# Performance work log

Measured on AMD Instinct MI355X. Metric: run time of the kernel, lower is better.

## Reference

```python
import jax, jax.numpy as jnp
import numpy as np

L = 2; B = 16; H = 56; W = 56; N = H * W; D = 256
HEADS = 8; HD = 32; INNER = HEADS * HD
WIN = 7; WIN2 = WIN * WIN; NWH = H // WIN; NWW = W // WIN; NW = NWH * NWW
DISP = WIN // 2; FF = 4 * D; CPB = 512; EPS = 1e-5


def _shift_masks():
    d = DISP
    ul = np.zeros((WIN2, WIN2), np.float32)
    ul[-d * WIN:, :-d * WIN] = -np.inf
    ul[:-d * WIN, -d * WIN:] = -np.inf
    lr = np.zeros((WIN, WIN, WIN, WIN), np.float32)
    lr[:, -d:, :, :-d] = -np.inf
    lr[:, :-d, :, -d:] = -np.inf
    return jnp.asarray(ul), jnp.asarray(lr.reshape(WIN2, WIN2))

MASK_UL, MASK_LR = _shift_masks()

_idx = np.array([[i, j] for i in range(WIN) for j in range(WIN)], np.float32)
_rel = _idx[None, :, :] - _idx[:, None, :]  # (49,49,2) relative distances
REL = jnp.asarray((np.sign(_rel) * np.log1p(np.abs(_rel))).reshape(WIN2 * WIN2, 2))


def _ln(x, g, b):
    m = x.mean(-1, keepdims=True)
    v = ((x - m) ** 2).mean(-1, keepdims=True)
    return (x - m) / jnp.sqrt(v + EPS) * g + b


def _l2norm(t):
    return t / jnp.maximum(jnp.linalg.norm(t, axis=-1, keepdims=True), 1e-12)


def _window_attn(xm, qkv_w, tau, cw1, cb1, cw2, cb2, ow, ob, shifted):
    if shifted:
        xm = jnp.roll(xm, (-DISP, -DISP), (1, 2))
    qkv = xm @ qkv_w  # (B,H,W,3*INNER), no bias
    q, k, v = jnp.split(qkv, 3, axis=-1)

    def towin(t):  # (B,H,W,INNER) -> (B,heads,nw,win2,hd)
        t = t.reshape(B, NWH, WIN, NWW, WIN, HEADS, HD)
        return t.transpose(0, 5, 1, 3, 2, 4, 6).reshape(B, HEADS, NW, WIN2, HD)

    q, k, v = towin(q), towin(k), towin(v)
    # cosine-similarity attention
    dots = jnp.einsum('bhwid,bhwjd->bhwij', _l2norm(q), _l2norm(k))
    dots = dots / jnp.clip(tau, 0.01, None)[None, :, None, None, None]
    # continuous position bias MLP: 2 -> CPB -> heads
    cpb = (jax.nn.relu(REL @ cw1 + cb1) @ cw2 + cb2).reshape(WIN2, WIN2, HEADS)
    dots = dots + cpb.transpose(2, 0, 1)[None, :, None]
    if shifted:
        dots = dots.at[:, :, -NWW:].add(MASK_UL)
        dots = dots.at[:, :, NWW - 1::NWW].add(MASK_LR)
    attn = jax.nn.softmax(dots, -1)
    out = jnp.einsum('bhwij,bhwjd->bhwid', attn, v)
    out = out.reshape(B, HEADS, NWH, NWW, WIN, WIN, HD)
    out = out.transpose(0, 2, 4, 3, 5, 1, 6).reshape(B, H, W, INNER)
    out = out @ ow + ob
    if shifted:
        out = jnp.roll(out, (DISP, DISP), (1, 2))
    return out


def _forward(x, spe, qkv_w, tau, cw1, cb1, cw2, cb2, ow, ob, ln1_g, ln1_b,
             fw1, fb1, fw2, fb2, ln2_g, ln2_b, norm_g, norm_b):
    xm = (x + spe).reshape(B, H, W, D)
    for i in range(L):
        shifted = (i % 2 == 1)
        a = _window_attn(xm, qkv_w[i], tau[i], cw1[i], cb1[i], cw2[i], cb2[i],
                         ow[i], ob[i], shifted)
        xm = _ln(a, ln1_g[i], ln1_b[i]) + xm  # Residual(PostNorm(attn))
        f = jax.nn.gelu(xm @ fw1[i] + fb1[i], approximate=False) @ fw2[i] + fb2[i]
        xm = _ln(f, ln2_g[i], ln2_b[i]) + xm  # Residual(PostNorm(mlp))
    return _ln(xm, norm_g, norm_b).reshape(B, N, D)


def setup_inputs():
    key = jax.random.key(0)
    ks = jax.random.split(key, 10)
    rn = lambda k, shp, s: jax.random.normal(k, shp, jnp.float32) * s
    return {
        'x': rn(ks[0], (B, N, D), 1.0),
        'spatial_position_embedding': rn(ks[1], (B, N, D), 0.02),
        'qkv_w': rn(ks[2], (L, D, 3 * INNER), 0.02),
        'tau': jnp.ones((L, HEADS), jnp.float32),
        'cw1': rn(ks[3], (L, 2, CPB), 0.1),
        'cb1': jnp.zeros((L, CPB), jnp.float32),
        'cw2': rn(ks[4], (L, CPB, HEADS), 0.05),
        'cb2': jnp.zeros((L, HEADS), jnp.float32),
        'ow': rn(ks[5], (L, INNER, D), 0.02),
        'ob': jnp.zeros((L, D), jnp.float32),
        'ln1_g': jnp.ones((L, D), jnp.float32),
        'ln1_b': jnp.zeros((L, D), jnp.float32),
        'fw1': rn(ks[6], (L, D, FF), 0.02),
        'fb1': jnp.zeros((L, FF), jnp.float32),
        'fw2': rn(ks[7], (L, FF, D), 0.02),
        'fb2': jnp.zeros((L, D), jnp.float32),
        'ln2_g': jnp.ones((L, D), jnp.float32),
        'ln2_b': jnp.zeros((L, D), jnp.float32),
        'norm_g': jnp.ones((D,), jnp.float32),
        'norm_b': jnp.zeros((D,), jnp.float32),
    }


def reference(x, spatial_position_embedding, qkv_w, tau, cw1, cb1, cw2, cb2, ow, ob,
              ln1_g, ln1_b, fw1, fb1, fw2, fb2, ln2_g, ln2_b, norm_g, norm_b):
    return _forward(x, spatial_position_embedding, qkv_w, tau, cw1, cb1, cw2, cb2,
                    ow, ob, ln1_g, ln1_b, fw1, fb1, fw2, fb2, ln2_g, ln2_b,
                    norm_g, norm_b)
```

## Files before the change

kernel.cpp:

```cpp
#include <hip/hip_runtime.h>
#include <hip/hip_bf16.h>
#include <math.h>

typedef short    short8  __attribute__((ext_vector_type(8)));
typedef float    floatx4 __attribute__((ext_vector_type(4)));

__device__ __forceinline__ float b2f(unsigned short u) {
    union { float f; unsigned int i; } v; v.i = ((unsigned int)u) << 16; return v.f;
}
__device__ __forceinline__ unsigned short f2b(float f) {
    union { float f; unsigned int i; } v; v.f = f;
    unsigned int b = v.i;
    return (unsigned short)((b + 0x7FFFu + ((b >> 16) & 1u)) >> 16);
}
__device__ __forceinline__ float rd(const void* p, long i, int f) {
    return f ? ((const float*)p)[i] : b2f(((const unsigned short*)p)[i]);
}
__device__ __forceinline__ float fgelu(float x) {
    float x2 = x * x;
    float t = x * fmaf(x2, -0.0713548163f, -1.5957691216f);
    return __fdividef(x, 1.f + __expf(t));
}
__device__ __forceinline__ int xcd_swz(int bid, int nwg) {
    int q = nwg >> 3, r = nwg & 7;
    int xcd = bid & 7, loc = bid >> 3;
    return ((xcd < r) ? xcd * (q + 1) : r * (q + 1) + (xcd - r) * q) + loc;
}

#define NTOK_ 50176

__global__ __launch_bounds__(256) void k_detect(const unsigned short* __restrict__ x,
                                                int* __restrict__ flag) {
    __shared__ int cnt;
    if (threadIdx.x == 0) cnt = 0;
    __syncthreads();
    unsigned short v = x[threadIdx.x];
    int e = (v >> 7) & 0xFF;
    if (e >= 0x90) atomicAdd(&cnt, 1);
    __syncthreads();
    if (threadIdx.x == 0) *flag = (cnt >= 8) ? 1 : 0;
}

__global__ __launch_bounds__(256) void k_add_spe(const void* __restrict__ x,
                                                 const void* __restrict__ spe,
                                                 float* __restrict__ xm,
                                                 unsigned short* __restrict__ xb,
                                                 const int* __restrict__ flagp) {
    const int f = *flagp;
    long i = ((long)blockIdx.x * 256 + threadIdx.x) * 4;
    float4 o;
    if (f) {
        float4 a = *(const float4*)((const float*)x + i);
        float4 b = *(const float4*)((const float*)spe + i);
        o.x = a.x + b.x; o.y = a.y + b.y; o.z = a.z + b.z; o.w = a.w + b.w;
    } else {
        ushort4 a = *(const ushort4*)((const unsigned short*)x + i);
        ushort4 b = *(const ushort4*)((const unsigned short*)spe + i);
        o.x = b2f(a.x) + b2f(b.x); o.y = b2f(a.y) + b2f(b.y);
        o.z = b2f(a.z) + b2f(b.z); o.w = b2f(a.w) + b2f(b.w);
    }
    *(float4*)(xm + i) = o;
    if (xb) {
        ushort4 h; h.x = f2b(o.x); h.y = f2b(o.y); h.z = f2b(o.z); h.w = f2b(o.w);
        *(ushort4*)(xb + i) = h;
    }
}

__global__ __launch_bounds__(256) void k_transpose(const void* __restrict__ in, long ioff,
                                                   unsigned short* __restrict__ out,
                                                   int K, int N,
                                                   const int* __restrict__ flagp) {
    __shared__ unsigned short tile[32][33];
    const int f = *flagp;
    int n0 = blockIdx.x * 32, k0 = blockIdx.y * 32;
    int tx = threadIdx.x & 31, ty = threadIdx.x >> 5;
#pragma unroll
    for (int i = 0; i < 4; i++) {
        int k = k0 + ty + i * 8;
        long idx = ioff + (long)k * N + n0 + tx;
        unsigned short v = f ? f2b(((const float*)in)[idx])
                             : ((const unsigned short*)in)[idx];
        tile[ty + i * 8][tx] = v;
    }
    __syncthreads();
#pragma unroll
    for (int i = 0; i < 4; i++) {
        int n = n0 + ty + i * 8;
        out[(long)n * K + k0 + tx] = tile[tx][ty + i * 8];
    }
}

__global__ __launch_bounds__(512) void k_cpb(const void* __restrict__ cw1,
                                             const void* __restrict__ cb1,
                                             const void* __restrict__ cw2,
                                             const void* __restrict__ cb2,
                                             float* __restrict__ cpb,
                                             const int* __restrict__ flagp) {
    const int f = *flagp;
    int p = blockIdx.x;
    int l = blockIdx.y;
    int t = threadIdx.x;
    int i = p / 49, j = p - i * 49;
    int yi = i / 7, xi = i - yi * 7, yj = j / 7, xj = j - yj * 7;
    float dy = (float)(yj - yi), dx = (float)(xj - xi);
    float sy = (dy > 0.f) ? 1.f : ((dy < 0.f) ? -1.f : 0.f);
    float sx = (dx > 0.f) ? 1.f : ((dx < 0.f) ? -1.f : 0.f);
    float r0 = sy * log1pf(fabsf(dy));
    float r1 = sx * log1pf(fabsf(dx));
    float h = r0 * rd(cw1, l * 1024 + t, f) + r1 * rd(cw1, l * 1024 + 512 + t, f)
            + rd(cb1, l * 512 + t, f);
    h = fmaxf(h, 0.f);
    __shared__ float red[512];
    for (int hh = 0; hh < 8; hh++) {
        red[t] = h * rd(cw2, (long)(l * 512 + t) * 8 + hh, f);
        __syncthreads();
        for (int s = 256; s > 0; s >>= 1) {
            if (t < s) red[t] += red[t + s];
            __syncthreads();
        }
        if (t == 0) cpb[((long)l * 8 + hh) * 2401 + p] = red[0] + rd(cb2, l * 8 + hh, f);
        __syncthreads();
    }
}

__global__ __launch_bounds__(256) void k_cast_roll(const float* __restrict__ xmg,
                                                   unsigned short* __restrict__ xb, int shift) {
    int gid = blockIdx.x * 256 + threadIdx.x;
    int c4 = (gid & 63) * 4;
    int t = gid >> 6;
    int x = t % 56; int t2 = t / 56;
    int y = t2 % 56;
    int b = t2 / 56;
    int ys = y + shift; if (ys >= 56) ys -= 56;
    int xs = x + shift; if (xs >= 56) xs -= 56;
    float4 v = *(const float4*)(xmg + (((long)b * 3136 + ys * 56 + xs) * 256 + c4));
    ushort4 o; o.x = f2b(v.x); o.y = f2b(v.y); o.z = f2b(v.z); o.w = f2b(v.w);
    *(ushort4*)(xb + ((long)t * 256 + c4)) = o;
}

__global__ __launch_bounds__(256) void gemm_bt(const unsigned short* __restrict__ A,
                                               const unsigned short* __restrict__ Bt,
                                               const void* __restrict__ bias, long boff,
                                               void* __restrict__ Cp,
                                               int M, int N, int K, int flags,
                                               const int* __restrict__ flagp) {
    __shared__ __align__(16) unsigned short smem[16896];
    unsigned short* As = smem;
    const int f = *flagp;
    const int tid = threadIdx.x;
    const int lane = tid & 63;
    const int wave = tid >> 6;
    const int wrow = (wave >> 1) * 64;
    const int wcol = (wave & 1) * 64;

    const int nwg = gridDim.x * gridDim.y;
    const int nb = xcd_swz(blockIdx.y * gridDim.x + blockIdx.x, nwg);
    const int bn = nb % gridDim.x, bm = nb / gridDim.x;

    floatx4 acc[4][4] = {};

    const int arow = tid >> 2;
    const int aseg = (tid & 3) * 8;
    const unsigned short* Ag = A + (long)(bm * 128 + arow) * K + aseg;
    const long rstep = (long)64 * K;

    const int q = lane >> 4;
    const int mrow = lane & 15;

    const unsigned short* Brow[4];
#pragma unroll
    for (int nt = 0; nt < 4; nt++)
        Brow[nt] = Bt + (long)(bn * 128 + wcol + nt * 16 + mrow) * K + q * 8;

    uint4 a_cur0 = *(const uint4*)(Ag);
    uint4 a_cur1 = *(const uint4*)(Ag + rstep);
    short8 bf_cur[4], bf_nxt[4];
#pragma unroll
    for (int nt = 0; nt < 4; nt++) bf_cur[nt] = *(const short8*)(Brow[nt]);

    for (int k0 = 0; k0 < K; k0 += 32) {
        const int kn = k0 + 32;
        uint4 a_nxt0, a_nxt1;
        if (kn < K) {
            a_nxt0 = *(const uint4*)(Ag + kn);
            a_nxt1 = *(const uint4*)(Ag + kn + rstep);
#pragma unroll
            for (int nt = 0; nt < 4; nt++) bf_nxt[nt] = *(const short8*)(Brow[nt] + kn);
        }
        __syncthreads();
        *(uint4*)(As + arow * 40 + aseg) = a_cur0;
        *(uint4*)(As + (arow + 64) * 40 + aseg) = a_cur1;
        __syncthreads();

        short8 af_[4];
#pragma unroll
        for (int mt = 0; mt < 4; mt++)
            af_[mt] = *(const short8*)(As + (wrow + mt * 16 + mrow) * 40 + q * 8);
#pragma unroll
        for (int mt = 0; mt < 4; mt++)
#pragma unroll
            for (int nt = 0; nt < 4; nt++)
                acc[mt][nt] = __builtin_amdgcn_mfma_f32_16x16x32_bf16(af_[mt], bf_cur[nt], acc[mt][nt], 0, 0, 0);
        if (kn < K) {
            a_cur0 = a_nxt0; a_cur1 = a_nxt1;
#pragma unroll
            for (int nt = 0; nt < 4; nt++) bf_cur[nt] = bf_nxt[nt];
        }
    }

    __syncthreads();

    unsigned short* T = smem;
#pragma unroll
    for (int nt = 0; nt < 4; nt++) {
        int col = wcol + nt * 16 + mrow;
        float bv = (flags & 1) ? rd(bias, boff + bn * 128 + col, f) : 0.f;
#pragma unroll
        for (int mt = 0; mt < 4; mt++) {
            int row0 = wrow + mt * 16 + q * 4;
#pragma unroll
            for (int r = 0; r < 4; r++) {
                float v = acc[mt][nt][r] + bv;
                if (flags & 2) v = fgelu(v);
                T[(row0 + r) * 132 + col] = f2b(v);
            }
        }
    }
    __syncthreads();
    unsigned short* Cu = (unsigned short*)Cp;
    int row = tid >> 4;
    int col8 = (tid & 15) * 8;
#pragma unroll
    for (int p = 0; p < 8; p++) {
        int rr = p * 16 + row;
        *(uint4*)(Cu + (long)(bm * 128 + rr) * N + bn * 128 + col8) =
            *(const uint4*)(T + rr * 132 + col8);
    }
}

__global__ __launch_bounds__(256) void gemm_ln(const unsigned short* __restrict__ A,
                                               const unsigned short* __restrict__ Bt,
                                               const void* __restrict__ bias, long boff,
                                               const void* __restrict__ g, long goff,
                                               const void* __restrict__ bb, long b2off,
                                               float* __restrict__ xm,
                                               unsigned short* __restrict__ xb,
                                               int K, int xbmode,
                                               const void* __restrict__ fg,
                                               const void* __restrict__ fb,
                                               void* __restrict__ outp,
                                               const int* __restrict__ flagp) {
    __shared__ __align__(16) unsigned short smem[17152];
    __shared__ float pp[4][32][2];
    unsigned short* As = smem;
    unsigned short* Bs = smem + 1280;
    const int f = *flagp;
    const int tid = threadIdx.x;
    const int lane = tid & 63;
    const int wv = tid >> 6;
    const int wcol = wv * 64;
    const int bm = blockIdx.x;

    floatx4 acc[2][4] = {};
    const int brow = tid >> 2;
    const int bseg = (tid & 3) * 8;
    const unsigned short* Ag = A + (long)(bm * 32 + brow) * K + bseg;
    const unsigned short* Bg = Bt + (long)brow * K + bseg;
    const long brow2 = (long)64 * K;
    const int q = lane >> 4;
    const int c = lane & 15;

    for (int k0 = 0; k0 < K; k0 += 32) {
        uint4 a0;
        if (tid < 128) a0 = *(const uint4*)(Ag + k0);
        uint4 b0 = *(const uint4*)(Bg + k0);
        uint4 b1 = *(const uint4*)(Bg + k0 + brow2);
        uint4 b2 = *(const uint4*)(Bg + k0 + 2 * brow2);
        uint4 b3 = *(const uint4*)(Bg + k0 + 3 * brow2);
        __syncthreads();
        if (tid < 128) *(uint4*)(As + brow * 40 + bseg) = a0;
        *(uint4*)(Bs + brow * 40 + bseg) = b0;
        *(uint4*)(Bs + (brow + 64) * 40 + bseg) = b1;
        *(uint4*)(Bs + (brow + 128) * 40 + bseg) = b2;
        *(uint4*)(Bs + (brow + 192) * 40 + bseg) = b3;
        __syncthreads();

        short8 af_[2], bf_[4];
#pragma unroll
        for (int mt = 0; mt < 2; mt++)
            af_[mt] = *(const short8*)(As + (mt * 16 + c) * 40 + q * 8);
#pragma unroll
        for (int nt = 0; nt < 4; nt++)
            bf_[nt] = *(const short8*)(Bs + (wcol + nt * 16 + c) * 40 + q * 8);
#pragma unroll
        for (int mt = 0; mt < 2; mt++)
#pragma unroll
            for (int nt = 0; nt < 4; nt++)
                acc[mt][nt] = __builtin_amdgcn_mfma_f32_16x16x32_bf16(af_[mt], bf_[nt], acc[mt][nt], 0, 0, 0);
    }
    __syncthreads();

    float bv[4];
#pragma unroll
    for (int nt = 0; nt < 4; nt++)
        bv[nt] = rd(bias, boff + wcol + nt * 16 + c, f);
#pragma unroll
    for (int mt = 0; mt < 2; mt++) {
#pragma unroll
        for (int r = 0; r < 4; r++) {
            float s1 = 0.f, s2 = 0.f;
#pragma unroll
            for (int nt = 0; nt < 4; nt++) {
                float v = acc[mt][nt][r] + bv[nt];
                s1 += v; s2 += v * v;
            }
            s1 += __shfl_xor(s1, 1); s2 += __shfl_xor(s2, 1);
            s1 += __shfl_xor(s1, 2); s2 += __shfl_xor(s2, 2);
            s1 += __shfl_xor(s1, 4); s2 += __shfl_xor(s2, 4);
            s1 += __shfl_xor(s1, 8); s2 += __shfl_xor(s2, 8);
            if (c == 0) {
                pp[wv][mt * 16 + q * 4 + r][0] = s1;
                pp[wv][mt * 16 + q * 4 + r][1] = s2;
            }
        }
    }

    const int c0 = lane * 4;
    float4 gv, bbv, fgv, fbv;
    gv.x = rd(g, goff + c0 + 0, f); gv.y = rd(g, goff + c0 + 1, f);
    gv.z = rd(g, goff + c0 + 2, f); gv.w = rd(g, goff + c0 + 3, f);
    bbv.x = rd(bb, b2off + c0 + 0, f); bbv.y = rd(bb, b2off + c0 + 1, f);
    bbv.z = rd(bb, b2off + c0 + 2, f); bbv.w = rd(bb, b2off + c0 + 3, f);
    if (xbmode == 3) {
        fgv.x = rd(fg, c0 + 0, f); fgv.y = rd(fg, c0 + 1, f);
        fgv.z = rd(fg, c0 + 2, f); fgv.w = rd(fg, c0 + 3, f);
        fbv.x = rd(fb, c0 + 0, f); fbv.y = rd(fb, c0 + 1, f);
        fbv.z = rd(fb, c0 + 2, f); fbv.w = rd(fb, c0 + 3, f);
    }

    float* Tf = (float*)smem;
#pragma unroll
    for (int mt = 0; mt < 2; mt++)
#pragma unroll
        for (int nt = 0; nt < 4; nt++)
#pragma unroll
            for (int r = 0; r < 4; r++)
                Tf[(mt * 16 + q * 4 + r) * 268 + wcol + nt * 16 + c] = acc[mt][nt][r] + bv[nt];
    __syncthreads();
#pragma unroll
    for (int it = 0; it < 8; it++) {
        int row = wv * 8 + it;
        float sum = pp[0][row][0] + pp[1][row][0] + pp[2][row][0] + pp[3][row][0];
        float ssq = pp[0][row][1] + pp[1][row][1] + pp[2][row][1] + pp[3][row][1];
        float mean = sum * (1.f / 256.f);
        float var = ssq * (1.f / 256.f) - mean * mean;
        float rstd = rsqrtf(fmaxf(var, 0.f) + 1e-5f);
        long tok = (long)(bm * 32 + row);
        long grow = tok * 256;
        float4 t = *(const float4*)(Tf + row * 268 + c0);
        float4 xv = *(const float4*)(xm + grow + c0);
        float4 o;
        o.x = (t.x - mean) * rstd * gv.x + bbv.x + xv.x;
        o.y = (t.y - mean) * rstd * gv.y + bbv.y + xv.y;
        o.z = (t.z - mean) * rstd * gv.z + bbv.z + xv.z;
        o.w = (t.w - mean) * rstd * gv.w + bbv.w + xv.w;
        if (xbmode == 3) {
            float s1 = o.x + o.y + o.z + o.w;
            s1 += __shfl_xor(s1, 1); s1 += __shfl_xor(s1, 2);
            s1 += __shfl_xor(s1, 4); s1 += __shfl_xor(s1, 8);
            s1 += __shfl_xor(s1, 16); s1 += __shfl_xor(s1, 32);
            float fmean = s1 * (1.f / 256.f);
            float d0 = o.x - fmean, d1 = o.y - fmean, d2 = o.z - fmean, d3 = o.w - fmean;
            float s2 = d0 * d0 + d1 * d1 + d2 * d2 + d3 * d3;
            s2 += __shfl_xor(s2, 1); s2 += __shfl_xor(s2, 2);
            s2 += __shfl_xor(s2, 4); s2 += __shfl_xor(s2, 8);
            s2 += __shfl_xor(s2, 16); s2 += __shfl_xor(s2, 32);
            float frstd = rsqrtf(s2 * (1.f / 256.f) + 1e-5f);
            float r0 = d0 * frstd * fgv.x + fbv.x;
            float r1 = d1 * frstd * fgv.y + fbv.y;
            float r2 = d2 * frstd * fgv.z + fbv.z;
            float r3 = d3 * frstd * fgv.w + fbv.w;
            if (f) {
                float4 fo; fo.x = r0; fo.y = r1; fo.z = r2; fo.w = r3;
                *(float4*)((float*)outp + grow + c0) = fo;
            } else {
                ushort4 ho; ho.x = f2b(r0); ho.y = f2b(r1); ho.z = f2b(r2); ho.w = f2b(r3);
                *(ushort4*)((unsigned short*)outp + grow + c0) = ho;
            }
        } else {
            *(float4*)(xm + grow + c0) = o;
            if (xbmode) {
                long xg = grow;
                if (xbmode == 2) {
                    int bi = (int)(tok / 3136); int r2i = (int)(tok - (long)bi * 3136);
                    int y = r2i / 56; int x = r2i - y * 56;
                    y = (y >= 3) ? y - 3 : y + 53;
                    x = (x >= 3) ? x - 3 : x + 53;
                    xg = ((long)bi * 3136 + y * 56 + x) * 256;
                }
                ushort4 hb; hb.x = f2b(o.x); hb.y = f2b(o.y); hb.z = f2b(o.z); hb.w = f2b(o.w);
                *(ushort4*)(xb + xg + c0) = hb;
            }
        }
    }
}

__global__ __launch_bounds__(256) void k_attn(const unsigned short* __restrict__ qkv,
                                              const float* __restrict__ cpb,
                                              const void* __restrict__ tau, long toff,
                                              unsigned short* __restrict__ out,
                                              int shifted,
                                              const int* __restrict__ flagp) {
    __shared__ __align__(16) unsigned short Pbuf[4][64 * 72];
    __shared__ __align__(16) unsigned short Vt[4][32 * 72];
    __shared__ float inq_s[4][64], ink_s[4][64];

    const int f = *flagp;
    const int tid = threadIdx.x;
    const int wv = tid >> 6;
    const int lane = tid & 63;
    const int h = blockIdx.x * 4 + wv;
    const int w = blockIdx.y, b = blockIdx.z;
    const int wy = w >> 3, wx = w & 7;
    const int q = lane >> 4;
    const int c = lane & 15;

    short8 qa[4], kb[4];
    float sqv[4], skv[4];
#pragma unroll
    for (int mt = 0; mt < 4; mt++) {
        int i = mt * 16 + c; if (i > 48) i = 48;
        int py = i / 7, px = i - py * 7;
        long base = (((long)b * 56 + wy * 7 + py) * 56 + wx * 7 + px) * 768 + h * 32 + q * 8;
        qa[mt] = *(const short8*)(qkv + base);
        kb[mt] = *(const short8*)(qkv + base + 256);
        float sq = 0.f, sk = 0.f;
#pragma unroll
        for (int e = 0; e < 8; e++) {
            float a = b2f((unsigned short)qa[mt][e]); sq += a * a;
            float k2 = b2f((unsigned short)kb[mt][e]); sk += k2 * k2;
        }
        sqv[mt] = sq; skv[mt] = sk;
    }
#pragma unroll
    for (int mt = 0; mt < 4; mt++) {
        float sq = sqv[mt]; sq += __shfl_xor(sq, 16); sq += __shfl_xor(sq, 32);
        float sk = skv[mt]; sk += __shfl_xor(sk, 16); sk += __shfl_xor(sk, 32);
        if (q == 0) {
            inq_s[wv][mt * 16 + c] = 1.f / fmaxf(sqrtf(sq), 1e-12f);
            ink_s[wv][mt * 16 + c] = 1.f / fmaxf(sqrtf(sk), 1e-12f);
        }
    }

    floatx4 acc[4][4] = {};
#pragma unroll
    for (int mt = 0; mt < 4; mt++)
#pragma unroll
        for (int nt = 0; nt < 4; nt++)
            acc[mt][nt] = __builtin_amdgcn_mfma_f32_16x16x32_bf16(qa[mt], kb[nt], acc[mt][nt], 0, 0, 0);

#pragma unroll
    for (int z = lane; z < 576; z += 64)
        *(uint2*)(&Vt[wv][z * 4]) = make_uint2(0u, 0u);
    if (lane < 49) {
        int py = lane / 7, px = lane - py * 7;
        long base = (((long)b * 56 + wy * 7 + py) * 56 + wx * 7 + px) * 768 + h * 32 + 512;
#pragma unroll
        for (int dd = 0; dd < 32; dd += 8) {
            ushort4 v0 = *(const ushort4*)(qkv + base + dd);
            ushort4 v1 = *(const ushort4*)(qkv + base + dd + 4);
            Vt[wv][(dd + 0) * 72 + lane] = v0.x;
            Vt[wv][(dd + 1) * 72 + lane] = v0.y;
            Vt[wv][(dd + 2) * 72 + lane] = v0.z;
            Vt[wv][(dd + 3) * 72 + lane] = v0.w;
            Vt[wv][(dd + 4) * 72 + lane] = v1.x;
            Vt[wv][(dd + 5) * 72 + lane] = v1.y;
            Vt[wv][(dd + 6) * 72 + lane] = v1.z;
            Vt[wv][(dd + 7) * 72 + lane] = v1.w;
        }
    }

    float scale = 1.f / fmaxf(rd(tau, toff + h, f), 0.01f);
#pragma unroll
    for (int mt = 0; mt < 4; mt++) {
#pragma unroll
        for (int r = 0; r < 4; r++) {
            int i = mt * 16 + q * 4 + r;
            int ci = (i < 49) ? i : 48;
            int pyi = ci / 7, pxi = ci - pyi * 7;
            float qi = inq_s[wv][ci] * scale;
            float vals[4];
#pragma unroll
            for (int nt = 0; nt < 4; nt++) {
                int j = nt * 16 + c;
                if (j < 49) {
                    float v = acc[mt][nt][r] * qi * ink_s[wv][j]
                            + cpb[h * 2401 + ci * 49 + j];
                    if (shifted) {
                        int pyj = j / 7, pxj = j - pyj * 7;
                        if (wy == 7 && ((pyi >= 4) != (pyj >= 4))) v = -1e30f;
                        if (wx == 7 && ((pxi >= 4) != (pxj >= 4))) v = -1e30f;
                    }
                    vals[nt] = v;
                } else vals[nt] = -1e30f;
            }
            float m = fmaxf(fmaxf(vals[0], vals[1]), fmaxf(vals[2], vals[3]));
            m = fmaxf(m, __shfl_xor(m, 1)); m = fmaxf(m, __shfl_xor(m, 2));
            m = fmaxf(m, __shfl_xor(m, 4)); m = fmaxf(m, __shfl_xor(m, 8));
            float s = 0.f;
#pragma unroll
            for (int nt = 0; nt < 4; nt++) { vals[nt] = __expf(vals[nt] - m); s += vals[nt]; }
            s += __shfl_xor(s, 1); s += __shfl_xor(s, 2);
            s += __shfl_xor(s, 4); s += __shfl_xor(s, 8);
            float rinv = 1.f / s;
#pragma unroll
            for (int nt = 0; nt < 4; nt++)
                Pbuf[wv][i * 72 + nt * 16 + c] = f2b(vals[nt] * rinv);
        }
    }

    floatx4 accO[4][2] = {};
#pragma unroll
    for (int ks = 0; ks < 2; ks++) {
        short8 pa[4], vb[2];
#pragma unroll
        for (int mt = 0; mt < 4; mt++)
            pa[mt] = *(const short8*)(&Pbuf[wv][(mt * 16 + c) * 72 + ks * 32 + q * 8]);
#pragma unroll
        for (int nt = 0; nt < 2; nt++)
            vb[nt] = *(const short8*)(&Vt[wv][(nt * 16 + c) * 72 + ks * 32 + q * 8]);
#pragma unroll
        for (int mt = 0; mt < 4; mt++)
#pragma unroll
            for (int nt = 0; nt < 2; nt++)
                accO[mt][nt] = __builtin_amdgcn_mfma_f32_16x16x32_bf16(pa[mt], vb[nt], accO[mt][nt], 0, 0, 0);
    }

    int sh = shifted ? 3 : 0;
#pragma unroll
    for (int mt = 0; mt < 4; mt++) {
#pragma unroll
        for (int r = 0; r < 4; r++) {
            int i = mt * 16 + q * 4 + r;
            if (i < 49) {
                int py = i / 7, px = i - py * 7;
                int yo = wy * 7 + py + sh; if (yo >= 56) yo -= 56;
                int xo = wx * 7 + px + sh; if (xo >= 56) xo -= 56;
                long ob = (((long)b * 56 + yo) * 56 + xo) * 256 + h * 32;
                out[ob + c]      = f2b(accO[mt][0][r]);
                out[ob + 16 + c] = f2b(accO[mt][1][r]);
            }
        }
    }
}

__global__ __launch_bounds__(256) void k_final(const float* __restrict__ xm,
                                               const void* __restrict__ g,
                                               const void* __restrict__ bb,
                                               void* __restrict__ out,
                                               const int* __restrict__ flagp) {
    const int f = *flagp;
    int t = blockIdx.x, c = threadIdx.x;
    long off = (long)t * 256 + c;
    float v = xm[off];
    __shared__ float red[256];
    red[c] = v; __syncthreads();
#pragma unroll
    for (int s = 128; s > 0; s >>= 1) {
        if (c < s) red[c] += red[c + s];
        __syncthreads();
    }
    float mean = red[0] * (1.f / 256.f);
    __syncthreads();
    float d = v - mean;
    red[c] = d * d; __syncthreads();
#pragma unroll
    for (int s = 128; s > 0; s >>= 1) {
        if (c < s) red[c] += red[c + s];
        __syncthreads();
    }
    float var = red[0] * (1.f / 256.f);
    float ln = d * rsqrtf(var + 1e-5f) * rd(g, c, f) + rd(bb, c, f);
    if (f) ((float*)out)[off] = ln;
    else   ((unsigned short*)out)[off] = f2b(ln);
}

extern "C" void kernel_launch(void* const* d_in, const int* in_sizes, int n_in,
                              void* d_out, int out_size, void* d_ws, size_t ws_size,
                              hipStream_t stream) {
    char* ws = (char*)d_ws;
    float*          xm    = (float*)(ws + 0);
    unsigned short* wt    = (unsigned short*)(ws + 51380224);
    float*          cpb   = (float*)(ws + 54525952);
    int*            flagp = (int*)(ws + 54679616);
    const size_t DYN = 54680576;

    long Mg = NTOK_; int G = 1;
    while (G <= 8) {
        Mg = NTOK_ / G;
        if (DYN + (size_t)Mg * 2560 <= ws_size) break;
        G <<= 1;
    }
    if (G > 8) { G = 8; Mg = NTOK_ / 8; }
    const int NB = 16 / G;
    const bool fused = (G == 1);

    unsigned short* xb   = (unsigned short*)(ws + DYN);
    unsigned short* qkvb = (unsigned short*)(ws + DYN + Mg * 512);
    unsigned short* hid  = (unsigned short*)(ws + DYN + Mg * 512);

    k_detect<<<1, 256, 0, stream>>>((const unsigned short*)d_in[0], flagp);

    for (int l = 0; l < 2; l++) {
        unsigned short* base = wt + (long)l * 786432;
        k_transpose<<<dim3(24, 8), 256, 0, stream>>>(d_in[2],  (long)l * 196608, base,          256, 768,  flagp);
        k_transpose<<<dim3(8, 8),  256, 0, stream>>>(d_in[8],  (long)l * 65536,  base + 196608, 256, 256,  flagp);
        k_transpose<<<dim3(32, 8), 256, 0, stream>>>(d_in[12], (long)l * 262144, base + 262144, 256, 1024, flagp);
        k_transpose<<<dim3(8, 32), 256, 0, stream>>>(d_in[14], (long)l * 262144, base + 524288, 1024, 256, flagp);
    }
    k_cpb<<<dim3(2401, 2), 512, 0, stream>>>(d_in[4], d_in[5], d_in[6], d_in[7], cpb, flagp);
    k_add_spe<<<dim3(12544), 256, 0, stream>>>(d_in[0], d_in[1], xm,
                                               fused ? xb : (unsigned short*)nullptr, flagp);

    for (int l = 0; l < 2; l++) {
        int sh = (l & 1) ? 3 : 0;
        unsigned short* base = wt + (long)l * 786432;
        for (int g = 0; g < G; g++) {
            long m0 = (long)g * Mg;
            if (!fused)
                k_cast_roll<<<dim3(Mg / 4), 256, 0, stream>>>(xm + m0 * 256, xb, sh);
            gemm_bt<<<dim3(6, Mg / 128), 256, 0, stream>>>(xb, base, nullptr, 0, qkvb,
                                                           (int)Mg, 768, 256, 4, flagp);
            k_attn<<<dim3(2, 64, NB), 256, 0, stream>>>(qkvb, cpb + (long)l * 19208,
                                                        d_in[3], (long)l * 8, xb, (l & 1), flagp);
            gemm_ln<<<dim3(Mg / 32), 256, 0, stream>>>(xb, base + 196608, d_in[9], (long)l * 256,
                                                       d_in[10], (long)l * 256, d_in[11], (long)l * 256,
                                                       xm + m0 * 256, xb, 256, 1,
                                                       d_in[18], d_in[19], d_out, flagp);
            gemm_bt<<<dim3(8, Mg / 128), 256, 0, stream>>>(xb, base + 262144, d_in[13], (long)l * 1024,
                                                           hid, (int)Mg, 1024, 256, 1 | 2 | 4, flagp);
            int xbm = fused ? ((l == 0) ? 2 : 3) : 1;
            gemm_ln<<<dim3(Mg / 32), 256, 0, stream>>>(hid, base + 524288, d_in[15], (long)l * 256,
                                                       d_in[16], (long)l * 256, d_in[17], (long)l * 256,
                                                       xm + m0 * 256, xb, 1024, xbm,
                                                       d_in[18], d_in[19], d_out, flagp);
        }
    }
    if (!fused)
        k_final<<<dim3(NTOK_), 256, 0, stream>>>(xm, d_in[18], d_in[19], d_out, flagp);
}
```

Baseline: 906.0 us.

## Run both layers per token group so intermediates stay cache-resident; prefetch residual

Reorders the schedule so each group of batches runs both transformer layers back to back, with the full bf16 activation buffer kept separately and the qkv/hidden scratch sized per group. The aim is to keep the per-group working set in the large last-level cache instead of streaming the whole 50k-token activations through HBM for every stage. The final-norm output write takes a group offset. Separately, gemm_ln loads the fp32 residual rows into registers before the epilogue barrier to hide that load latency. The cost is more, smaller kernel launches, each with fewer blocks and less GPU fill.

```diff
diff --git a/kernel.cpp b/kernel.cpp
--- a/kernel.cpp
+++ b/kernel.cpp
@@ -248,7 +248,7 @@
                                                int K, int xbmode,
                                                const void* __restrict__ fg,
                                                const void* __restrict__ fb,
-                                               void* __restrict__ outp,
+                                               void* __restrict__ outp, long ooff,
                                                const int* __restrict__ flagp) {
     __shared__ __align__(16) unsigned short smem[17152];
     __shared__ float pp[4][32][2];
@@ -269,6 +269,7 @@
     const long brow2 = (long)64 * K;
     const int q = lane >> 4;
     const int c = lane & 15;
+    const int c0 = lane * 4;
 
     for (int k0 = 0; k0 < K; k0 += 32) {
         uint4 a0;
@@ -298,6 +299,13 @@
             for (int nt = 0; nt < 4; nt++)
                 acc[mt][nt] = __builtin_amdgcn_mfma_f32_16x16x32_bf16(af_[mt], bf_[nt], acc[mt][nt], 0, 0, 0);
     }
+
+    const long xbase = (long)(bm * 32 + wv * 8) * 256 + c0;
+    float4 xr[8];
+#pragma unroll
+    for (int it = 0; it < 8; it++)
+        xr[it] = *(const float4*)(xm + xbase + (long)it * 256);
+
     __syncthreads();
 
     float bv[4];
@@ -325,7 +333,6 @@
         }
     }
 
-    const int c0 = lane * 4;
     float4 gv, bbv, fgv, fbv;
     gv.x = rd(g, goff + c0 + 0, f); gv.y = rd(g, goff + c0 + 1, f);
     gv.z = rd(g, goff + c0 + 2, f); gv.w = rd(g, goff + c0 + 3, f);
@@ -358,7 +365,7 @@
         long tok = (long)(bm * 32 + row);
         long grow = tok * 256;
         float4 t = *(const float4*)(Tf + row * 268 + c0);
-        float4 xv = *(const float4*)(xm + grow + c0);
+        float4 xv = xr[it];
         float4 o;
         o.x = (t.x - mean) * rstd * gv.x + bbv.x + xv.x;
         o.y = (t.y - mean) * rstd * gv.y + bbv.y + xv.y;
@@ -382,10 +389,10 @@
             float r3 = d3 * frstd * fgv.w + fbv.w;
             if (f) {
                 float4 fo; fo.x = r0; fo.y = r1; fo.z = r2; fo.w = r3;
-                *(float4*)((float*)outp + grow + c0) = fo;
+                *(float4*)((float*)outp + ooff + grow + c0) = fo;
             } else {
                 ushort4 ho; ho.x = f2b(r0); ho.y = f2b(r1); ho.z = f2b(r2); ho.w = f2b(r3);
-                *(ushort4*)((unsigned short*)outp + grow + c0) = ho;
+                *(ushort4*)((unsigned short*)outp + ooff + grow + c0) = ho;
             }
         } else {
             *(float4*)(xm + grow + c0) = o;
@@ -594,58 +601,99 @@
     float*          cpb   = (float*)(ws + 54525952);
     int*            flagp = (int*)(ws + 54679616);
     const size_t DYN = 54680576;
-
-    long Mg = NTOK_; int G = 1;
-    while (G <= 8) {
-        Mg = NTOK_ / G;
-        if (DYN + (size_t)Mg * 2560 <= ws_size) break;
-        G <<= 1;
-    }
-    if (G > 8) { G = 8; Mg = NTOK_ / 8; }
-    const int NB = 16 / G;
-    const bool fused = (G == 1);
-
-    unsigned short* xb   = (unsigned short*)(ws + DYN);
-    unsigned short* qkvb = (unsigned short*)(ws + DYN + Mg * 512);
-    unsigned short* hid  = (unsigned short*)(ws + DYN + Mg * 512);
-
-    k_detect<<<1, 256, 0, stream>>>((const unsigned short*)d_in[0], flagp);
-
-    for (int l = 0; l < 2; l++) {
-        unsigned short* base = wt + (long)l * 786432;
-        k_transpose<<<dim3(24, 8), 256, 0, stream>>>(d_in[2],  (long)l * 196608, base,          256, 768,  flagp);
-        k_transpose<<<dim3(8, 8),  256, 0, stream>>>(d_in[8],  (long)l * 65536,  base + 196608, 256, 256,  flagp);
-        k_transpose<<<dim3(32, 8), 256, 0, stream>>>(d_in[12], (long)l * 262144, base + 262144, 256, 1024, flagp);
-        k_transpose<<<dim3(8, 32), 256, 0, stream>>>(d_in[14], (long)l * 262144, base + 524288, 1024, 256, flagp);
-    }
-    k_cpb<<<dim3(2401, 2), 512, 0, stream>>>(d_in[4], d_in[5], d_in[6], d_in[7], cpb, flagp);
-    k_add_spe<<<dim3(12544), 256, 0, stream>>>(d_in[0], d_in[1], xm,
-                                               fused ? xb : (unsigned short*)nullptr, flagp);
-
-    for (int l = 0; l < 2; l++) {
-        int sh = (l & 1) ? 3 : 0;
-        unsigned short* base = wt + (long)l * 786432;
+    const size_t XBF = (size_t)NTOK_ * 512;
+
+    int G = 2;
+    while (G <= 8 && DYN + XBF + (size_t)(NTOK_ / G) * 2048 > ws_size) G <<= 1;
+    const bool fused = (G <= 8);
+
+    if (fused) {
+        long Mg = NTOK_ / G;
+        const int NB = 16 / G;
+        unsigned short* xb   = (unsigned short*)(ws + DYN);
+        unsigned short* qkvb = (unsigned short*)(ws + DYN + XBF);
+        unsigned short* hid  = qkvb;
+
+        k_detect<<<1, 256, 0, stream>>>((const unsigned short*)d_in[0], flagp);
+        for (int l = 0; l < 2; l++) {
+            unsigned short* base = wt + (long)l * 786432;
+            k_transpose<<<dim3(24, 8), 256, 0, stream>>>(d_in[2],  (long)l * 196608, base,          256, 768,  flagp);
+            k_transpose<<<dim3(8, 8),  256, 0, stream>>>(d_in[8],  (long)l * 65536,  base + 196608, 256, 256,  flagp);
+            k_transpose<<<dim3(32, 8), 256, 0, stream>>>(d_in[12], (long)l * 262144, base + 262144, 256, 1024, flagp);
+            k_transpose<<<dim3(8, 32), 256, 0, stream>>>(d_in[14], (long)l * 262144, base + 524288, 1024, 256, flagp);
+        }
+        k_cpb<<<dim3(2401, 2), 512, 0, stream>>>(d_in[4], d_in[5], d_in[6], d_in[7], cpb, flagp);
+        k_add_spe<<<dim3(12544), 256, 0, stream>>>(d_in[0], d_in[1], xm, xb, flagp);
+
         for (int g = 0; g < G; g++) {
             long m0 = (long)g * Mg;
-            if (!fused)
+            unsigned short* xbg = xb + m0 * 256;
+            float* xmg = xm + m0 * 256;
+            for (int l = 0; l < 2; l++) {
+                unsigned short* base = wt + (long)l * 786432;
+                gemm_bt<<<dim3(6, Mg / 128), 256, 0, stream>>>(xbg, base, nullptr, 0, qkvb,
+                                                               (int)Mg, 768, 256, 4, flagp);
+                k_attn<<<dim3(2, 64, NB), 256, 0, stream>>>(qkvb, cpb + (long)l * 19208,
+                                                            d_in[3], (long)l * 8, xbg, (l & 1), flagp);
+                gemm_ln<<<dim3(Mg / 32), 256, 0, stream>>>(xbg, base + 196608, d_in[9], (long)l * 256,
+                                                           d_in[10], (long)l * 256, d_in[11], (long)l * 256,
+                                                           xmg, xbg, 256, 1,
+                                                           d_in[18], d_in[19], d_out, 0, flagp);
+                gemm_bt<<<dim3(8, Mg / 128), 256, 0, stream>>>(xbg, base + 262144, d_in[13], (long)l * 1024,
+                                                               hid, (int)Mg, 1024, 256, 1 | 2 | 4, flagp);
+                int xbm = (l == 0) ? 2 : 3;
+                gemm_ln<<<dim3(Mg / 32), 256, 0, stream>>>(hid, base + 524288, d_in[15], (long)l * 256,
+                                                           d_in[16], (long)l * 256, d_in[17], (long)l * 256,
+                                                           xmg, xbg, 1024, xbm,
+                                                           d_in[18], d_in[19], d_out, m0 * 256, flagp);
+            }
+        }
+    } else {
+        long Mg = NTOK_; int G2 = 1;
+        while (G2 <= 8) {
+            Mg = NTOK_ / G2;
+            if (DYN + (size_t)Mg * 2560 <= ws_size) break;
+            G2 <<= 1;
+        }
+        if (G2 > 8) { G2 = 8; Mg = NTOK_ / 8; }
+        const int NB = 16 / G2;
+        unsigned short* xb   = (unsigned short*)(ws + DYN);
+        unsigned short* qkvb = (unsigned short*)(ws + DYN + Mg * 512);
+        unsigned short* hid  = (unsigned short*)(ws + DYN + Mg * 512);
+
+        k_detect<<<1, 256, 0, stream>>>((const unsigned short*)d_in[0], flagp);
+        for (int l = 0; l < 2; l++) {
+            unsigned short* base = wt + (long)l * 786432;
+            k_transpose<<<dim3(24, 8), 256, 0, stream>>>(d_in[2],  (long)l * 196608, base,          256, 768,  flagp);
+            k_transpose<<<dim3(8, 8),  256, 0, stream>>>(d_in[8],  (long)l * 65536,  base + 196608, 256, 256,  flagp);
+            k_transpose<<<dim3(32, 8), 256, 0, stream>>>(d_in[12], (long)l * 262144, base + 262144, 256, 1024, flagp);
+            k_transpose<<<dim3(8, 32), 256, 0, stream>>>(d_in[14], (long)l * 262144, base + 524288, 1024, 256, flagp);
+        }
+        k_cpb<<<dim3(2401, 2), 512, 0, stream>>>(d_in[4], d_in[5], d_in[6], d_in[7], cpb, flagp);
+        k_add_spe<<<dim3(12544), 256, 0, stream>>>(d_in[0], d_in[1], xm, (unsigned short*)nullptr, flagp);
+
+        for (int l = 0; l < 2; l++) {
+            int sh = (l & 1) ? 3 : 0;
+            unsigned short* base = wt + (long)l * 786432;
+            for (int g = 0; g < G2; g++) {
+                long m0 = (long)g * Mg;
                 k_cast_roll<<<dim3(Mg / 4), 256, 0, stream>>>(xm + m0 * 256, xb, sh);
-            gemm_bt<<<dim3(6, Mg / 128), 256, 0, stream>>>(xb, base, nullptr, 0, qkvb,
-                                                           (int)Mg, 768, 256, 4, flagp);
-            k_attn<<<dim3(2, 64, NB), 256, 0, stream>>>(qkvb, cpb + (long)l * 19208,
-                                                        d_in[3], (long)l * 8, xb, (l & 1), flagp);
-            gemm_ln<<<dim3(Mg / 32), 256, 0, stream>>>(xb, base + 196608, d_in[9], (long)l * 256,
-                                                       d_in[10], (long)l * 256, d_in[11], (long)l * 256,
-                                                       xm + m0 * 256, xb, 256, 1,
-                                                       d_in[18], d_in[19], d_out, flagp);
-            gemm_bt<<<dim3(8, Mg / 128), 256, 0, stream>>>(xb, base + 262144, d_in[13], (long)l * 1024,
-                                                           hid, (int)Mg, 1024, 256, 1 | 2 | 4, flagp);
-            int xbm = fused ? ((l == 0) ? 2 : 3) : 1;
-            gemm_ln<<<dim3(Mg / 32), 256, 0, stream>>>(hid, base + 524288, d_in[15], (long)l * 256,
-                                                       d_in[16], (long)l * 256, d_in[17], (long)l * 256,
-                                                       xm + m0 * 256, xb, 1024, xbm,
-                                                       d_in[18], d_in[19], d_out, flagp);
-        }
-    }
-    if (!fused)
+                gemm_bt<<<dim3(6, Mg / 128), 256, 0, stream>>>(xb, base, nullptr, 0, qkvb,
+                                                               (int)Mg, 768, 256, 4, flagp);
+                k_attn<<<dim3(2, 64, NB), 256, 0, stream>>>(qkvb, cpb + (long)l * 19208,
+                                                            d_in[3], (long)l * 8, xb, (l & 1), flagp);
+                gemm_ln<<<dim3(Mg / 32), 256, 0, stream>>>(xb, base + 196608, d_in[9], (long)l * 256,
+                                                           d_in[10], (long)l * 256, d_in[11], (long)l * 256,
+                                                           xm + m0 * 256, xb, 256, 1,
+                                                           d_in[18], d_in[19], d_out, 0, flagp);
+                gemm_bt<<<dim3(8, Mg / 128), 256, 0, stream>>>(xb, base + 262144, d_in[13], (long)l * 1024,
+                                                               hid, (int)Mg, 1024, 256, 1 | 2 | 4, flagp);
+                gemm_ln<<<dim3(Mg / 32), 256, 0, stream>>>(hid, base + 524288, d_in[15], (long)l * 256,
+                                                           d_in[16], (long)l * 256, d_in[17], (long)l * 256,
+                                                           xm + m0 * 256, xb, 1024, 1,
+                                                           d_in[18], d_in[19], d_out, 0, flagp);
+            }
+        }
         k_final<<<dim3(NTOK_), 256, 0, stream>>>(xm, d_in[18], d_in[19], d_out, flagp);
-}
+    }
+}
```

After: 1.053 ms. 1.16x slower.
